# Kernel optimization log

Hardware: AMD Instinct MI355X
Metric: run time of the kernel (lower is better)

Reference implementation:

```python
import jax, jax.numpy as jnp
import numpy as np

NEG = -1e30


def setup_inputs() -> dict:
    key = jax.random.key(0)
    k1, k2, k3, k4 = jax.random.split(key, 4)
    B, L, T, M = 64, 256, 1600, 80
    probs = jax.random.uniform(k1, (B, L, T), dtype=jnp.float32)
    melspec = jax.random.normal(k2, (B, M, T), dtype=jnp.float32)
    text_lengths = jax.random.randint(k3, (B,), 1, L + 1)   # values in [1, L]
    mel_lengths = jax.random.randint(k4, (B,), 1, T + 1)    # values in [1, T]
    return {"probs": probs, "melspec": melspec,
            "text_lengths": text_lengths, "mel_lengths": mel_lengths}


def reference(probs, melspec, text_lengths, mel_lengths):
    B, L, _ = probs.shape
    T = melspec.shape[2]
    log_prob_matrix = jnp.log(probs + 1e-30)            # [B, L, T]
    lp_t = jnp.moveaxis(log_prob_matrix, 2, 0)          # [T, B, L]

    # t = 0: only (l=0, t=0) is alive
    init = jnp.full((B, L), NEG, dtype=log_prob_matrix.dtype)
    init = init.at[:, 0].set(lp_t[0, :, 0])

    def step(prev, lp):
        # stay at label l, or advance from label l-1 (monotonic alignment)
        shifted = jnp.concatenate(
            [jnp.full((B, 1), NEG, dtype=prev.dtype), prev[:, :-1]], axis=1)
        new = jnp.logaddexp(prev, shifted) + lp
        return new, new

    _, ys = jax.lax.scan(step, init, lp_t[1:])          # ys: [T-1, B, L]
    log_alpha = jnp.concatenate([init[None], ys], axis=0)  # [T, B, L]

    b = jnp.arange(B)
    alpha_last = log_alpha[mel_lengths - 1, b, text_lengths - 1]  # [B]
    mdn_loss = -alpha_last.mean()
    return (mdn_loss, log_prob_matrix)
```

## Files before the change

kernel.cpp:

```cpp
#include <hip/hip_runtime.h>

#define LN2f 0.69314718055994531f

constexpr int CK   = 8;
constexpr int PD   = 3;
constexpr int DP_B = 64;
constexpr int T_C  = 1600;
constexpr int L_C  = 256;
constexpr int NCH  = T_C / CK;

__global__ __launch_bounds__(256, 1) void fused_kernel(
    const float* __restrict__ probs,
    const int* __restrict__ text_len,
    const int* __restrict__ mel_len,
    float* __restrict__ out1,
    float* __restrict__ alpha_out,
    int n4, int G)
{
    const int b   = blockIdx.x;
    const int tid = threadIdx.x;

    if (b < DP_B && tid < 64) {
        asm volatile("s_setprio 3");
        const int lane = tid;
        const float* rr[4];
        rr[0] = probs + ((size_t)b * L_C + lane * 4) * T_C;
        rr[1] = rr[0] + T_C;
        rr[2] = rr[1] + T_C;
        rr[3] = rr[2] + T_C;
        const int ml1 = mel_len[b] - 1;
        const int cl  = text_len[b] - 1;

        float a0 = 0.f, a1 = 0.f, a2 = 0.f, a3 = 0.f;
        int   E = 0;
        bool  alive = (lane == 0);
        float s0 = 0.f, s1 = 0.f, s2 = 0.f, s3 = 0.f;
        int   sE = 0;

        float4 buf[PD][4][2];

        auto loadc = [&](int slot, int ck) {
            int tb = ck * CK;
#pragma unroll
            for (int r = 0; r < 4; ++r) {
                buf[slot][r][0] = *(const float4*)(rr[r] + tb);
                buf[slot][r][1] = *(const float4*)(rr[r] + tb + 4);
            }
        };

        auto getc = [&](int slot, int r, int j) -> float {
            const float4 v = buf[slot][r][j >> 2];
            const int q = j & 3;
            return ((q == 0) ? v.x : (q == 1) ? v.y : (q == 2) ? v.z : v.w) + 1e-30f;
        };

        auto step_full = [&](float c0, float c1, float c2, float c3, int t) {
            float top = __shfl_up(a3, 1, 64);
            int   tE  = __shfl_up(E, 1, 64);
            top = (lane == 0) ? 0.0f : top;
            float contrib = alive ? ldexpf(top, tE - E) : top;
            E = alive ? E : tE;
            alive = alive | (top != 0.0f);
            float n0 = (a0 + contrib) * c0;
            float n1 = (a1 + a0) * c1;
            float n2 = (a2 + a1) * c2;
            float n3 = (a3 + a2) * c3;
            a0 = n0; a1 = n1; a2 = n2; a3 = n3;
            if (t == ml1) { s0 = a0; s1 = a1; s2 = a2; s3 = a3; sE = E; }
        };

        auto renorm = [&]() {
            float m = fmaxf(fmaxf(a0, a1), fmaxf(a2, a3));
            int e = ((__float_as_int(m) >> 23) & 255) - 127;
            e = (m > 0.0f) ? e : 0;
            a0 = ldexpf(a0, -e); a1 = ldexpf(a1, -e);
            a2 = ldexpf(a2, -e); a3 = ldexpf(a3, -e);
            E += e;
        };

        auto proc_full = [&](int slot, int ck) {
            const int tb = ck * CK;
#pragma unroll
            for (int j = 0; j < CK; ++j)
                step_full(getc(slot, 0, j), getc(slot, 1, j),
                          getc(slot, 2, j), getc(slot, 3, j), tb + j);
            renorm();
            loadc(slot, ck + PD);
        };

        auto proc_fast = [&](int slot, int ck) {
            int tE = __shfl_up(E, 1, 64);
            int dE = tE - E;
            const int tb = ck * CK;
#pragma unroll
            for (int j = 0; j < CK; ++j) {
                const float c0 = getc(slot, 0, j), c1 = getc(slot, 1, j);
                const float c2 = getc(slot, 2, j), c3 = getc(slot, 3, j);
                float top = __shfl_up(a3, 1, 64);
                top = (lane == 0) ? 0.0f : top;
                float contrib = ldexpf(top, dE);
                float n0 = (a0 + contrib) * c0;
                float n1 = (a1 + a0) * c1;
                float n2 = (a2 + a1) * c2;
                float n3 = (a3 + a2) * c3;
                a0 = n0; a1 = n1; a2 = n2; a3 = n3;
                if (tb + j == ml1) { s0 = a0; s1 = a1; s2 = a2; s3 = a3; sE = E; }
            }
            renorm();
            if (ck + PD < NCH) loadc(slot, ck + PD);
        };

        loadc(0, 0); loadc(1, 1); loadc(2, 2);

        {
            a0 = (lane == 0) ? getc(0, 0, 0) : 0.0f;
            if (ml1 == 0) { s0 = a0; s1 = 0.f; s2 = 0.f; s3 = 0.f; sE = 0; }
#pragma unroll
            for (int j = 1; j < CK; ++j)
                step_full(getc(0, 0, j), getc(0, 1, j), getc(0, 2, j), getc(0, 3, j), j);
            renorm();
            loadc(0, PD);
        }

        for (int g = 0; g < 10; ++g) {
            const int ck = 1 + 3 * g;
            proc_full(1, ck); proc_full(2, ck + 1); proc_full(0, ck + 2);
        }
        proc_full(1, 31);
        proc_full(2, 32);

        for (int g = 0; g < 55; ++g) {
            const int ck = 33 + 3 * g;
            proc_fast(0, ck); proc_fast(1, ck + 1); proc_fast(2, ck + 2);
        }
        proc_fast(0, 198);
        proc_fast(1, 199);

        if (lane == (cl >> 2)) {
            const int jj = cl & 3;
            float v = (jj == 0) ? s0 : (jj == 1) ? s1 : (jj == 2) ? s2 : s3;
            v = fmaxf(v, 1e-44f);
            float res = (log2f(v) + (float)sE) * LN2f;
            alpha_out[b] = (cl > ml1) ? -1e30f : res;
        }
        return;
    }

    int widx;
    if (b < DP_B) widx = b * 192 + (tid - 64);
    else          widx = DP_B * 192 + (b - DP_B) * 256 + tid;
    const int W = DP_B * 192 + (G - DP_B) * 256;

    for (int i = widx; i < n4; i += W) {
        const float4 v = ((const float4*)probs)[i];
        const int o = 4 * i;
        out1[o + 0] = logf(v.x + 1e-30f);
        out1[o + 1] = logf(v.y + 1e-30f);
        out1[o + 2] = logf(v.z + 1e-30f);
        out1[o + 3] = logf(v.w + 1e-30f);
    }
}

__global__ void loss_kernel(const float* __restrict__ alpha,
                            float* __restrict__ out, int B) {
    float v = (threadIdx.x < B) ? alpha[threadIdx.x] : 0.0f;
#pragma unroll
    for (int off = 32; off > 0; off >>= 1) v += __shfl_down(v, off, 64);
    if (threadIdx.x == 0) out[0] = -v / (float)B;
}

extern "C" void kernel_launch(void* const* d_in, const int* in_sizes, int n_in,
                              void* d_out, int out_size, void* d_ws, size_t ws_size,
                              hipStream_t stream) {
    const float* probs    = (const float*)d_in[0];
    const int*   text_len = (const int*)d_in[2];
    const int*   mel_len  = (const int*)d_in[3];
    float* out = (float*)d_out;

    const int B  = in_sizes[2];
    const int n  = in_sizes[0];
    const int n4 = n / 4;
    const int G  = 1024;

    fused_kernel<<<G, 256, 0, stream>>>(probs, text_len, mel_len,
                                        out + 1, (float*)d_ws, n4, G);
    loss_kernel<<<1, 64, 0, stream>>>((const float*)d_ws, out, B);
}
```

Before: 312.5 us.

## Stage DP inputs via LDS producer waves, use DPP shifts, and stop at mel length

The DP block now uses three producer waves that load probability chunks from global memory into a double-buffered, swizzled LDS tile. The single DP wave reads from LDS and replaces __shfl_up with DPP row shifts plus cross-row broadcasts. The recursion stops after the chunk containing mel_length instead of running all 1600 steps. The log-output blocks become dedicated blocks using __logf with a software-prefetched next load. Risks include sync overhead per 32-step chunk, slightly less accurate fast log, and correctness of the DPP shift emulation across rows.

```diff
diff --git a/kernel.cpp b/kernel.cpp
--- a/kernel.cpp
+++ b/kernel.cpp
@@ -2,12 +2,29 @@
 
 #define LN2f 0.69314718055994531f
 
-constexpr int CK   = 8;
-constexpr int PD   = 3;
-constexpr int DP_B = 64;
 constexpr int T_C  = 1600;
 constexpr int L_C  = 256;
-constexpr int NCH  = T_C / CK;
+constexpr int DP_B = 64;
+constexpr int CK   = 32;
+constexpr int LOGB = 960;
+
+__device__ __forceinline__ float shift_up1_f(float x, bool f15, bool f31) {
+    int xi  = __float_as_int(x);
+    int s   = __builtin_amdgcn_update_dpp(0, xi, 0x111, 0xF, 0xF, true);
+    int b15 = __builtin_amdgcn_update_dpp(0, xi, 0x142, 0xF, 0xF, true);
+    int b31 = __builtin_amdgcn_update_dpp(0, xi, 0x143, 0xF, 0xF, true);
+    int r = f15 ? b15 : s;
+    r     = f31 ? b31 : r;
+    return __int_as_float(r);
+}
+__device__ __forceinline__ int shift_up1_i(int x, bool f15, bool f31) {
+    int s   = __builtin_amdgcn_update_dpp(0, x, 0x111, 0xF, 0xF, true);
+    int b15 = __builtin_amdgcn_update_dpp(0, x, 0x142, 0xF, 0xF, true);
+    int b31 = __builtin_amdgcn_update_dpp(0, x, 0x143, 0xF, 0xF, true);
+    int r = f15 ? b15 : s;
+    r     = f31 ? b31 : r;
+    return r;
+}
 
 __global__ __launch_bounds__(256, 1) void fused_kernel(
     const float* __restrict__ probs,
@@ -15,149 +32,177 @@
     const int* __restrict__ mel_len,
     float* __restrict__ out1,
     float* __restrict__ alpha_out,
-    int n4, int G)
+    int n4)
 {
+    __shared__ float lds[2][CK][L_C];
     const int b   = blockIdx.x;
     const int tid = threadIdx.x;
 
-    if (b < DP_B && tid < 64) {
-        asm volatile("s_setprio 3");
-        const int lane = tid;
-        const float* rr[4];
-        rr[0] = probs + ((size_t)b * L_C + lane * 4) * T_C;
-        rr[1] = rr[0] + T_C;
-        rr[2] = rr[1] + T_C;
-        rr[3] = rr[2] + T_C;
-        const int ml1 = mel_len[b] - 1;
-        const int cl  = text_len[b] - 1;
-
-        float a0 = 0.f, a1 = 0.f, a2 = 0.f, a3 = 0.f;
-        int   E = 0;
-        bool  alive = (lane == 0);
-        float s0 = 0.f, s1 = 0.f, s2 = 0.f, s3 = 0.f;
-        int   sE = 0;
-
-        float4 buf[PD][4][2];
-
-        auto loadc = [&](int slot, int ck) {
-            int tb = ck * CK;
-#pragma unroll
-            for (int r = 0; r < 4; ++r) {
-                buf[slot][r][0] = *(const float4*)(rr[r] + tb);
-                buf[slot][r][1] = *(const float4*)(rr[r] + tb + 4);
-            }
-        };
-
-        auto getc = [&](int slot, int r, int j) -> float {
-            const float4 v = buf[slot][r][j >> 2];
-            const int q = j & 3;
-            return ((q == 0) ? v.x : (q == 1) ? v.y : (q == 2) ? v.z : v.w) + 1e-30f;
-        };
-
-        auto step_full = [&](float c0, float c1, float c2, float c3, int t) {
-            float top = __shfl_up(a3, 1, 64);
-            int   tE  = __shfl_up(E, 1, 64);
-            top = (lane == 0) ? 0.0f : top;
+    if (b >= DP_B) {
+        const int W = LOGB * 256;
+        int i = (b - DP_B) * 256 + tid;
+        if (i >= n4) return;
+        const float4* p4 = (const float4*)probs;
+        float4 v = p4[i];
+        for (;;) {
+            const int  nx   = i + W;
+            const bool more = nx < n4;
+            float4 vn;
+            if (more) vn = p4[nx];
+            const int o = 4 * i;
+            out1[o + 0] = __logf(v.x + 1e-30f);
+            out1[o + 1] = __logf(v.y + 1e-30f);
+            out1[o + 2] = __logf(v.z + 1e-30f);
+            out1[o + 3] = __logf(v.w + 1e-30f);
+            if (!more) return;
+            v = vn; i = nx;
+        }
+    }
+
+    const int wv   = tid >> 6;
+    const int lane = tid & 63;
+    const int ml1  = mel_len[b] - 1;
+    const int trip = (ml1 >> 5) + 1;
+
+    if (wv != 0) {
+        asm volatile("s_setprio 1");
+        const int  pw   = wv - 1;
+        const int  f0   = pw * 64 + lane;
+        const int  q    = f0 & 7;
+        const int  row0 = f0 >> 3;
+        const bool lok  = pw < 2;
+        const float* gbase = probs + (size_t)b * (L_C * T_C)
+                           + (size_t)row0 * T_C + q * 4;
+        const int swz0 = 8 * (q & 3);
+        const int a0q  = q * 1024;
+
+        float4 rA[11], rB[11];
+        auto LD = [&](float4 (&r)[11], int ck) {
+            const float* p = gbase + ck * CK;
+#pragma unroll
+            for (int it = 0; it < 11; ++it)
+                if (it < 10 || lok)
+                    r[it] = *(const float4*)(p + it * (24 * T_C));
+        };
+        auto WR = [&](float4 (&r)[11], int bb) {
+            float* Lw = &lds[bb][0][0];
+#pragma unroll
+            for (int it = 0; it < 11; ++it) {
+                if (it < 10 || lok) {
+                    const int rw = (row0 + 24 * it) ^ swz0;
+                    const int A0 = a0q + rw;
+                    Lw[A0]             = r[it].x + 1e-30f;
+                    Lw[A0 + 256]       = r[it].y + 1e-30f;
+                    Lw[(A0 ^ 4) + 512] = r[it].z + 1e-30f;
+                    Lw[(A0 ^ 4) + 768] = r[it].w + 1e-30f;
+                }
+            }
+        };
+
+        LD(rA, 0);
+        if (trip > 1) LD(rB, 1);
+        WR(rA, 0);
+        for (int w = 0; w < trip; ++w) {
+            __syncthreads();
+            if ((w & 1) == 0) {
+                if (w + 2 < trip) LD(rA, w + 2);
+                if (w + 1 < trip) WR(rB, 1);
+            } else {
+                if (w + 2 < trip) LD(rB, w + 2);
+                if (w + 1 < trip) WR(rA, 0);
+            }
+        }
+        return;
+    }
+
+    asm volatile("s_setprio 3");
+    const int  cl  = text_len[b] - 1;
+    const bool f15 = (lane == 16) | (lane == 48);
+    const bool f31 = (lane == 32);
+    const int  xr  = 4 * lane;
+
+    float a0 = 0.f, a1 = 0.f, a2 = 0.f, a3 = 0.f;
+    int   E = 0;
+    bool  alive = (lane == 0);
+    float s0 = 0.f, s1 = 0.f, s2 = 0.f, s3 = 0.f;
+    int   sE = 0;
+
+    auto renorm = [&]() {
+        float m = fmaxf(fmaxf(a0, a1), fmaxf(a2, a3));
+        int e = ((__float_as_int(m) >> 23) & 255) - 127;
+        e = (m > 0.0f) ? e : 0;
+        a0 = ldexpf(a0, -e); a1 = ldexpf(a1, -e);
+        a2 = ldexpf(a2, -e); a3 = ldexpf(a3, -e);
+        E += e;
+    };
+
+    for (int w = 0; w < trip; ++w) {
+        __syncthreads();
+        const float* Lr = &lds[w & 1][0][0];
+        const int tb = w << 5;
+
+        auto ldc = [&](int j) -> float4 {
+            return *(const float4*)(Lr + j * 256 + (xr ^ (4 * ((j >> 1) & 7))));
+        };
+        auto step_full = [&](int j) {
+            const float4 c = ldc(j);
+            float top = shift_up1_f(a3, f15, f31);
+            int   tE  = shift_up1_i(E, f15, f31);
             float contrib = alive ? ldexpf(top, tE - E) : top;
             E = alive ? E : tE;
             alive = alive | (top != 0.0f);
-            float n0 = (a0 + contrib) * c0;
-            float n1 = (a1 + a0) * c1;
-            float n2 = (a2 + a1) * c2;
-            float n3 = (a3 + a2) * c3;
+            float n0 = (a0 + contrib) * c.x;
+            float n1 = (a1 + a0) * c.y;
+            float n2 = (a2 + a1) * c.z;
+            float n3 = (a3 + a2) * c.w;
             a0 = n0; a1 = n1; a2 = n2; a3 = n3;
-            if (t == ml1) { s0 = a0; s1 = a1; s2 = a2; s3 = a3; sE = E; }
-        };
-
-        auto renorm = [&]() {
-            float m = fmaxf(fmaxf(a0, a1), fmaxf(a2, a3));
-            int e = ((__float_as_int(m) >> 23) & 255) - 127;
-            e = (m > 0.0f) ? e : 0;
-            a0 = ldexpf(a0, -e); a1 = ldexpf(a1, -e);
-            a2 = ldexpf(a2, -e); a3 = ldexpf(a3, -e);
-            E += e;
-        };
-
-        auto proc_full = [&](int slot, int ck) {
-            const int tb = ck * CK;
-#pragma unroll
-            for (int j = 0; j < CK; ++j)
-                step_full(getc(slot, 0, j), getc(slot, 1, j),
-                          getc(slot, 2, j), getc(slot, 3, j), tb + j);
-            renorm();
-            loadc(slot, ck + PD);
-        };
-
-        auto proc_fast = [&](int slot, int ck) {
-            int tE = __shfl_up(E, 1, 64);
-            int dE = tE - E;
-            const int tb = ck * CK;
+            if (tb + j == ml1) { s0 = a0; s1 = a1; s2 = a2; s3 = a3; sE = E; }
+        };
+
+        if (w == 0) {
+            const float4 c = ldc(0);
+            a0 = (lane == 0) ? c.x : 0.0f;
+            if (ml1 == 0) s0 = a0;
+#pragma unroll
+            for (int j = 1; j < CK; ++j) {
+                step_full(j);
+                if ((j & 15) == 15) renorm();
+            }
+        } else if (w < 8) {
 #pragma unroll
             for (int j = 0; j < CK; ++j) {
-                const float c0 = getc(slot, 0, j), c1 = getc(slot, 1, j);
-                const float c2 = getc(slot, 2, j), c3 = getc(slot, 3, j);
-                float top = __shfl_up(a3, 1, 64);
-                top = (lane == 0) ? 0.0f : top;
-                float contrib = ldexpf(top, dE);
-                float n0 = (a0 + contrib) * c0;
-                float n1 = (a1 + a0) * c1;
-                float n2 = (a2 + a1) * c2;
-                float n3 = (a3 + a2) * c3;
-                a0 = n0; a1 = n1; a2 = n2; a3 = n3;
-                if (tb + j == ml1) { s0 = a0; s1 = a1; s2 = a2; s3 = a3; sE = E; }
-            }
-            renorm();
-            if (ck + PD < NCH) loadc(slot, ck + PD);
-        };
-
-        loadc(0, 0); loadc(1, 1); loadc(2, 2);
-
-        {
-            a0 = (lane == 0) ? getc(0, 0, 0) : 0.0f;
-            if (ml1 == 0) { s0 = a0; s1 = 0.f; s2 = 0.f; s3 = 0.f; sE = 0; }
-#pragma unroll
-            for (int j = 1; j < CK; ++j)
-                step_full(getc(0, 0, j), getc(0, 1, j), getc(0, 2, j), getc(0, 3, j), j);
-            renorm();
-            loadc(0, PD);
+                step_full(j);
+                if ((j & 15) == 15) renorm();
+            }
+        } else {
+#pragma unroll
+            for (int h = 0; h < 2; ++h) {
+                const int tE = shift_up1_i(E, f15, f31);
+                const int dE = tE - E;
+#pragma unroll
+                for (int jj = 0; jj < 16; ++jj) {
+                    const int j = h * 16 + jj;
+                    const float4 c = ldc(j);
+                    float top = shift_up1_f(a3, f15, f31);
+                    float contrib = ldexpf(top, dE);
+                    float n0 = (a0 + contrib) * c.x;
+                    float n1 = (a1 + a0) * c.y;
+                    float n2 = (a2 + a1) * c.z;
+                    float n3 = (a3 + a2) * c.w;
+                    a0 = n0; a1 = n1; a2 = n2; a3 = n3;
+                    if (tb + j == ml1) { s0 = a0; s1 = a1; s2 = a2; s3 = a3; sE = E; }
+                }
+                renorm();
+            }
         }
-
-        for (int g = 0; g < 10; ++g) {
-            const int ck = 1 + 3 * g;
-            proc_full(1, ck); proc_full(2, ck + 1); proc_full(0, ck + 2);
-        }
-        proc_full(1, 31);
-        proc_full(2, 32);
-
-        for (int g = 0; g < 55; ++g) {
-            const int ck = 33 + 3 * g;
-            proc_fast(0, ck); proc_fast(1, ck + 1); proc_fast(2, ck + 2);
-        }
-        proc_fast(0, 198);
-        proc_fast(1, 199);
-
-        if (lane == (cl >> 2)) {
-            const int jj = cl & 3;
-            float v = (jj == 0) ? s0 : (jj == 1) ? s1 : (jj == 2) ? s2 : s3;
-            v = fmaxf(v, 1e-44f);
-            float res = (log2f(v) + (float)sE) * LN2f;
-            alpha_out[b] = (cl > ml1) ? -1e30f : res;
-        }
-        return;
-    }
-
-    int widx;
-    if (b < DP_B) widx = b * 192 + (tid - 64);
-    else          widx = DP_B * 192 + (b - DP_B) * 256 + tid;
-    const int W = DP_B * 192 + (G - DP_B) * 256;
-
-    for (int i = widx; i < n4; i += W) {
-        const float4 v = ((const float4*)probs)[i];
-        const int o = 4 * i;
-        out1[o + 0] = logf(v.x + 1e-30f);
-        out1[o + 1] = logf(v.y + 1e-30f);
-        out1[o + 2] = logf(v.z + 1e-30f);
-        out1[o + 3] = logf(v.w + 1e-30f);
+    }
+
+    if (lane == (cl >> 2)) {
+        const int jj = cl & 3;
+        float v = (jj == 0) ? s0 : (jj == 1) ? s1 : (jj == 2) ? s2 : s3;
+        v = fmaxf(v, 1e-44f);
+        const float res = (log2f(v) + (float)sE) * LN2f;
+        alpha_out[b] = (cl > ml1) ? -1e30f : res;
     }
 }
 
@@ -180,9 +225,9 @@
     const int B  = in_sizes[2];
     const int n  = in_sizes[0];
     const int n4 = n / 4;
-    const int G  = 1024;
+    const int G  = DP_B + LOGB;
 
     fused_kernel<<<G, 256, 0, stream>>>(probs, text_len, mel_len,
-                                        out + 1, (float*)d_ws, n4, G);
+                                        out + 1, (float*)d_ws, n4);
     loss_kernel<<<1, 64, 0, stream>>>((const float*)d_ws, out, B);
 }
```

New measurement: 264.3 us. 1.18x faster.
